# Performance work log

Measured on AMD Instinct MI355X. Metric: run time of the kernel, lower is better.

Reference implementation:

```python
import jax, jax.numpy as jnp
import numpy as np


def gcn_conv(x, W, b, src, dst):
    """PyG-style GCNConv: add self-loops, symmetric normalization, then scatter-add."""
    n = x.shape[0]
    loop = jnp.arange(n, dtype=src.dtype)
    s = jnp.concatenate([src, loop])  # [E+N]
    d = jnp.concatenate([dst, loop])
    deg = jax.ops.segment_sum(jnp.ones(s.shape[0], dtype=x.dtype), d, num_segments=n)
    dinv = jax.lax.rsqrt(jnp.maximum(deg, 1.0))  # deg >= 1 due to self-loops
    norm = dinv[s] * dinv[d]                     # [E+N]
    h = x @ W                                    # [N, out]
    msg = h[s] * norm[:, None]                   # gather + scale
    return jax.ops.segment_sum(msg, d, num_segments=n) + b


def setup_inputs() -> dict:
    key = jax.random.key(0)
    ks = jax.random.split(key, 8)
    N, E, IN, H, C = 50000, 800000, 128, 64, 16
    x = jax.random.normal(ks[0], (N, IN), dtype=jnp.float32)
    edge_index = jax.random.randint(ks[1], (2, E), 0, N, dtype=jnp.int32)
    def glorot(k, shp):
        fan_in, fan_out = shp
        lim = (6.0 / (fan_in + fan_out)) ** 0.5
        return jax.random.uniform(k, shp, jnp.float32, -lim, lim)
    return {
        "x": x,
        "edge_index": edge_index,
        "W1": glorot(ks[2], (IN, H)), "b1": jnp.zeros((H,), jnp.float32),
        "W2": glorot(ks[3], (H, H)),  "b2": jnp.zeros((H,), jnp.float32),
        "Wm1": glorot(ks[4], (2 * H, H)), "bm1": jnp.zeros((H,), jnp.float32),
        "Wm2": glorot(ks[5], (H, C)),     "bm2": jnp.zeros((C,), jnp.float32),
    }


def reference(x, edge_index, W1, b1, W2, b2, Wm1, bm1, Wm2, bm2):
    src, dst = edge_index[0], edge_index[1]
    h = jax.nn.relu(gcn_conv(x, W1, b1, src, dst))
    # dropout is identity in eval mode
    h = jax.nn.relu(gcn_conv(h, W2, b2, src, dst))
    ef = jnp.concatenate([h[src], h[dst]], axis=1)  # [E, 2H]
    z = jax.nn.relu(ef @ Wm1 + bm1)
    return z @ Wm2 + bm2  # [E, numClasses]
```

## Files before the change

### kernel.cpp

```cpp
#include <hip/hip_runtime.h>
#include <hip/hip_bf16.h>

__global__ __launch_bounds__(256) void k_deg(const int* __restrict__ dst, int* __restrict__ deg, int E) {
    int e = blockIdx.x * 256 + threadIdx.x;
    if (e < E) atomicAdd(&deg[dst[e]], 1);
}

__global__ __launch_bounds__(256) void k_scan_sum(const int* __restrict__ deg, int* __restrict__ bsum,
                                                  float* __restrict__ dinv, int N) {
    int n = blockIdx.x * 256 + threadIdx.x;
    int v = (n < N) ? deg[n] : 0;
    if (n < N) dinv[n] = rsqrtf((float)(v + 1));
    int r = v;
#pragma unroll
    for (int o = 32; o > 0; o >>= 1) r += __shfl_down(r, o, 64);
    __shared__ int sh[4];
    if ((threadIdx.x & 63) == 0) sh[threadIdx.x >> 6] = r;
    __syncthreads();
    if (threadIdx.x == 0) bsum[blockIdx.x] = sh[0] + sh[1] + sh[2] + sh[3];
}

__global__ __launch_bounds__(256) void k_scan_off(int* __restrict__ bsum, int nb) {
    __shared__ int sh[256];
    int t = threadIdx.x;
    sh[t] = (t < nb) ? bsum[t] : 0;
    __syncthreads();
    for (int o = 1; o < 256; o <<= 1) {
        int y = (t >= o) ? sh[t - o] : 0;
        __syncthreads();
        sh[t] += y;
        __syncthreads();
    }
    if (t < nb) bsum[t] = (t == 0) ? 0 : sh[t - 1];
}

__global__ __launch_bounds__(256) void k_scan_write(const int* __restrict__ deg, const int* __restrict__ boff,
                                                    int* __restrict__ row_start, int* __restrict__ cursor, int N) {
    int n = blockIdx.x * 256 + threadIdx.x;
    int t = threadIdx.x, lane = t & 63, w = t >> 6;
    int v = (n < N) ? deg[n] : 0;
    int x = v;
#pragma unroll
    for (int o = 1; o < 64; o <<= 1) {
        int y = __shfl_up(x, o, 64);
        if (lane >= o) x += y;
    }
    __shared__ int wsum[4];
    if (lane == 63) wsum[w] = x;
    __syncthreads();
    int wo = 0;
#pragma unroll
    for (int i = 0; i < 4; ++i) wo += (i < w) ? wsum[i] : 0;
    int excl = boff[blockIdx.x] + wo + x - v;
    if (n < N) { row_start[n] = excl; cursor[n] = excl; }
    if (n == N - 1) row_start[N] = excl + v;
}

template <bool PAIR>
__global__ __launch_bounds__(256) void k_fill(const int* __restrict__ src, const int* __restrict__ dst,
                                              int* __restrict__ cursor, void* __restrict__ item, int E) {
    int e = blockIdx.x * 256 + threadIdx.x;
    if (e < E) {
        int d = dst[e];
        int pos = atomicAdd(&cursor[d], 1);
        if (PAIR) ((int2*)item)[pos] = make_int2(src[e], e);
        else      ((int*)item)[pos] = e;
    }
}

__global__ __launch_bounds__(256) void k_dvec(const int* __restrict__ rowst, int* __restrict__ dvec, int N) {
    int w = threadIdx.x >> 6, lane = threadIdx.x & 63;
    int d = blockIdx.x * 4 + w;
    if (d >= N) return;
    int beg = rowst[d], end = rowst[d + 1];
    for (int k = beg + lane; k < end; k += 64) dvec[k] = d;
}

__global__ __launch_bounds__(256) void k_prep(const float* __restrict__ W1, const float* __restrict__ W2,
                                              const float* __restrict__ Wm2, const float* __restrict__ Wm1,
                                              float* __restrict__ W1T, float* __restrict__ W2T,
                                              float* __restrict__ Wm2T, float* __restrict__ WPQ,
                                              int IN, int H) {
    int i = blockIdx.x * 256 + threadIdx.x;
    int n1 = IN * H, n2 = H * H, n3 = H * 16, n4 = 2 * H * H;
    if (i < n1) {
        int r = i / H, c = i % H;
        W1T[(size_t)c * IN + r] = W1[(size_t)r * H + c];
    } else if ((i -= n1) < n2) {
        int r = i / H, c = i % H;
        W2T[(size_t)c * H + r] = W2[(size_t)r * H + c];
    } else if ((i -= n2) < n3) {
        int r = i / 16, c = i % 16;
        Wm2T[(size_t)c * H + r] = Wm2[(size_t)r * 16 + c];
    } else if ((i -= n3) < n4) {
        int j = i >> 6, k = i & 63;
        WPQ[i] = (j < 64) ? Wm1[k * 64 + j] : Wm1[(64 + k) * 64 + (j - 64)];
    }
}

template <int K, bool RELU, bool BIAS, bool SCALE>
__global__ __launch_bounds__(256) void k_mm_slice(const float* __restrict__ X,
                                                  const float* __restrict__ WT,
                                                  const float* __restrict__ bias,
                                                  const float* __restrict__ dinv,
                                                  float* __restrict__ Y, int N) {
    int n = blockIdx.x * 256 + threadIdx.x;
    int j0 = blockIdx.y * 16;
    int nc = n < N ? n : N - 1;
    const float* xr = X + (size_t)nc * K;
    const float* wr = WT + (size_t)j0 * K;
    float acc[16];
#pragma unroll
    for (int j = 0; j < 16; ++j) acc[j] = BIAS ? bias[j0 + j] : 0.f;
#pragma unroll 1
    for (int k0 = 0; k0 < K; k0 += 8) {
        float ef[8];
        *(float4*)(ef)     = *(const float4*)(xr + k0);
        *(float4*)(ef + 4) = *(const float4*)(xr + k0 + 4);
        if (RELU) {
#pragma unroll
            for (int kk = 0; kk < 8; ++kk) ef[kk] = fmaxf(ef[kk], 0.f);
        }
#pragma unroll
        for (int j = 0; j < 16; ++j) {
#pragma unroll
            for (int kk = 0; kk < 8; ++kk)
                acc[j] = fmaf(ef[kk], wr[j * K + k0 + kk], acc[j]);
        }
    }
    if (n < N) {
        if (SCALE) {
            float dn = dinv[n];
#pragma unroll
            for (int j = 0; j < 16; ++j) acc[j] *= dn;
        }
        float4* yp = (float4*)(Y + (size_t)n * 64 + j0);
#pragma unroll
        for (int q = 0; q < 4; ++q) yp[q] = *(float4*)(acc + q * 4);
    }
}

__global__ __launch_bounds__(256) void k_pq_slice(const float* __restrict__ A2,
                                                  const float* __restrict__ WPQ,
                                                  const float* __restrict__ bm1,
                                                  float* __restrict__ Pb, float* __restrict__ Qb, int N) {
    int n = blockIdx.x * 256 + threadIdx.x;
    int j0g = blockIdx.y * 16;
    bool isP = j0g < 64;
    int jo = isP ? j0g : j0g - 64;
    float* Y = isP ? Pb : Qb;
    int nc = n < N ? n : N - 1;
    const float* xr = A2 + (size_t)nc * 64;
    const float* wr = WPQ + (size_t)j0g * 64;
    float acc[16];
#pragma unroll
    for (int j = 0; j < 16; ++j) acc[j] = isP ? bm1[jo + j] : 0.f;
#pragma unroll 1
    for (int k0 = 0; k0 < 64; k0 += 8) {
        float ef[8];
        *(float4*)(ef)     = *(const float4*)(xr + k0);
        *(float4*)(ef + 4) = *(const float4*)(xr + k0 + 4);
#pragma unroll
        for (int kk = 0; kk < 8; ++kk) ef[kk] = fmaxf(ef[kk], 0.f);
#pragma unroll
        for (int j = 0; j < 16; ++j)
#pragma unroll
            for (int kk = 0; kk < 8; ++kk)
                acc[j] = fmaf(ef[kk], wr[j * 64 + k0 + kk], acc[j]);
    }
    if (n < N) {
        float4* yp = (float4*)(Y + (size_t)n * 64 + jo);
#pragma unroll
        for (int q = 0; q < 4; ++q) yp[q] = *(float4*)(acc + q * 4);
    }
}

template <bool PAIR>
__global__ __launch_bounds__(256) void k_gather(const float* __restrict__ hs, const float* __restrict__ dinv,
                                                const int* __restrict__ row_start, const void* __restrict__ item,
                                                const int* __restrict__ srcArr,
                                                const float* __restrict__ bias,
                                                float* __restrict__ a, int N) {
    int w = threadIdx.x >> 6, lane = threadIdx.x & 63;
    int d = blockIdx.x * 4 + w;
    if (d >= N) return;
    int beg = row_start[d], end = row_start[d + 1];
    float dd = dinv[d];
    float acc = hs[(size_t)d * 64 + lane];
    int k = beg;
    for (; k + 16 <= end; k += 16) {
        int ss[16];
        if (PAIR) {
            const int2* it = (const int2*)item;
#pragma unroll
            for (int u = 0; u < 16; ++u) ss[u] = it[k + u].x;
        } else {
            const int* eid = (const int*)item;
            int ee[16];
#pragma unroll
            for (int u = 0; u < 16; ++u) ee[u] = eid[k + u];
#pragma unroll
            for (int u = 0; u < 16; ++u) ss[u] = srcArr[ee[u]];
        }
        float v[16];
#pragma unroll
        for (int u = 0; u < 16; ++u) v[u] = hs[(size_t)ss[u] * 64 + lane];
#pragma unroll
        for (int u = 0; u < 16; ++u) acc += v[u];
    }
    for (; k + 8 <= end; k += 8) {
        int ss[8];
        if (PAIR) {
            const int2* it = (const int2*)item;
#pragma unroll
            for (int u = 0; u < 8; ++u) ss[u] = it[k + u].x;
        } else {
            const int* eid = (const int*)item;
            int ee[8];
#pragma unroll
            for (int u = 0; u < 8; ++u) ee[u] = eid[k + u];
#pragma unroll
            for (int u = 0; u < 8; ++u) ss[u] = srcArr[ee[u]];
        }
        float v[8];
#pragma unroll
        for (int u = 0; u < 8; ++u) v[u] = hs[(size_t)ss[u] * 64 + lane];
#pragma unroll
        for (int u = 0; u < 8; ++u) acc += v[u];
    }
    for (; k < end; ++k) {
        int s = PAIR ? ((const int2*)item)[k].x : srcArr[((const int*)item)[k]];
        acc += hs[(size_t)s * 64 + lane];
    }
    a[(size_t)d * 64 + lane] = fmaf(acc, dd, bias[lane]);
}

__global__ __launch_bounds__(256) void k_p_inplace(float* __restrict__ A2P,
                                                   const float* __restrict__ WPQ,
                                                   const float* __restrict__ bm1, int N) {
    int n = blockIdx.x * 256 + threadIdx.x;
    int nc = n < N ? n : N - 1;
    const float* xr = A2P + (size_t)nc * 64;
    float acc[64];
#pragma unroll
    for (int j = 0; j < 64; ++j) acc[j] = bm1[j];
#pragma unroll 1
    for (int k0 = 0; k0 < 64; k0 += 8) {
        float ef[8];
        *(float4*)(ef)     = *(const float4*)(xr + k0);
        *(float4*)(ef + 4) = *(const float4*)(xr + k0 + 4);
#pragma unroll
        for (int kk = 0; kk < 8; ++kk) ef[kk] = fmaxf(ef[kk], 0.f);
#pragma unroll
        for (int j = 0; j < 64; ++j)
#pragma unroll
            for (int kk = 0; kk < 8; ++kk)
                acc[j] = fmaf(ef[kk], WPQ[j * 64 + k0 + kk], acc[j]);
    }
    if (n < N) {
#pragma unroll
        for (int q = 0; q < 16; ++q)
            *(float4*)(A2P + (size_t)n * 64 + q * 4) = *(float4*)(acc + q * 4);
    }
}

__global__ __launch_bounds__(256) void k_edge_pq(const float* __restrict__ P,
                                                 const float* __restrict__ Q,
                                                 const int* __restrict__ src,
                                                 const int* __restrict__ dst,
                                                 const float* __restrict__ W2T,
                                                 const float* __restrict__ bm2,
                                                 float* __restrict__ out, int E) {
    int e = blockIdx.x * 256 + threadIdx.x;
    int ec = e < E ? e : E - 1;
    int s = src[ec], d = dst[ec];
    const float4* p4 = (const float4*)(P + (size_t)s * 64);
    const float4* q4 = (const float4*)(Q + (size_t)d * 64);
    float z[64];
#pragma unroll
    for (int c = 0; c < 16; ++c) {
        float4 a = p4[c], b = q4[c];
        z[c * 4 + 0] = fmaxf(a.x + b.x, 0.f);
        z[c * 4 + 1] = fmaxf(a.y + b.y, 0.f);
        z[c * 4 + 2] = fmaxf(a.z + b.z, 0.f);
        z[c * 4 + 3] = fmaxf(a.w + b.w, 0.f);
    }
    float o[16];
#pragma unroll
    for (int c = 0; c < 16; ++c) {
        float a = bm2[c];
#pragma unroll
        for (int j = 0; j < 64; ++j) a = fmaf(z[j], W2T[c * 64 + j], a);
        o[c] = a;
    }
    if (e < E) {
        float4* op = (float4*)(out + (size_t)e * 16);
#pragma unroll
        for (int q = 0; q < 4; ++q) op[q] = *(float4*)(o + q * 4);
    }
}

template <bool PAIR>
__global__ __launch_bounds__(256) void k_edge_csr(const float* __restrict__ P,
                                                  const float* __restrict__ Q,
                                                  const int* __restrict__ dvec,
                                                  const void* __restrict__ item,
                                                  const int* __restrict__ srcArr,
                                                  const float* __restrict__ W2T,
                                                  const float* __restrict__ bm2,
                                                  float* __restrict__ out, int E) {
    int i = blockIdx.x * 256 + threadIdx.x;
    int ic = i < E ? i : E - 1;
    int s, e;
    if (PAIR) {
        int2 pe = ((const int2*)item)[ic];
        s = pe.x; e = pe.y;
    } else {
        e = ((const int*)item)[ic];
        s = srcArr[e];
    }
    int d = dvec[ic];
    const float4* p4 = (const float4*)(P + (size_t)s * 64);
    const float4* q4 = (const float4*)(Q + (size_t)d * 64);
    float o[16];
#pragma unroll
    for (int t = 0; t < 16; ++t) o[t] = bm2[t];
#pragma unroll
    for (int cc = 0; cc < 16; ++cc) {
        float4 a = p4[cc], b = q4[cc];
        float z0 = fmaxf(a.x + b.x, 0.f);
        float z1 = fmaxf(a.y + b.y, 0.f);
        float z2 = fmaxf(a.z + b.z, 0.f);
        float z3 = fmaxf(a.w + b.w, 0.f);
#pragma unroll
        for (int t = 0; t < 16; ++t) {
            o[t] = fmaf(z0, W2T[t * 64 + cc * 4 + 0], o[t]);
            o[t] = fmaf(z1, W2T[t * 64 + cc * 4 + 1], o[t]);
            o[t] = fmaf(z2, W2T[t * 64 + cc * 4 + 2], o[t]);
            o[t] = fmaf(z3, W2T[t * 64 + cc * 4 + 3], o[t]);
        }
    }
    if (i < E) {
        float4* op = (float4*)(out + (size_t)e * 16);
#pragma unroll
        for (int q = 0; q < 4; ++q) op[q] = *(float4*)(o + q * 4);
    }
}

extern "C" void kernel_launch(void* const* d_in, const int* in_sizes, int n_in,
                              void* d_out, int out_size, void* d_ws, size_t ws_size,
                              hipStream_t stream) {
    const float* x   = (const float*)d_in[0];
    const int* ei    = (const int*)d_in[1];
    const float* W1  = (const float*)d_in[2];
    const float* b1  = (const float*)d_in[3];
    const float* W2  = (const float*)d_in[4];
    const float* b2  = (const float*)d_in[5];
    const float* Wm1 = (const float*)d_in[6];
    const float* bm1 = (const float*)d_in[7];
    const float* Wm2 = (const float*)d_in[8];
    const float* bm2 = (const float*)d_in[9];
    float* out = (float*)d_out;

    const int H  = in_sizes[3];
    const int IN = in_sizes[2] / H;
    const int N  = in_sizes[0] / IN;
    const int E  = in_sizes[1] / 2;
    const int* src = ei;
    const int* dst = ei + E;

    auto al = [](size_t b) { return (b + 255) & ~(size_t)255; };
    char* ws = (char*)d_ws;

    const size_t wb     = al((size_t)IN * H * 4) + al((size_t)H * H * 4) + al((size_t)2 * H * H * 4) + al((size_t)H * 16 * 4);
    const size_t rowstB = al(((size_t)N + 1) * 4);
    const size_t nodeB  = al((size_t)N * 64 * 4);
    const size_t pairB  = al((size_t)E * 8);
    const size_t eidB   = al((size_t)E * 4);
    const size_t needA  = wb + rowstB + pairB + 3 * nodeB;
    const size_t needB  = wb + rowstB + eidB  + 3 * nodeB;

    const int tier = (needA <= ws_size) ? 0 : (needB <= ws_size) ? 1 : 2;

    float *W1T, *W2T, *WPQ, *Wm2T, *bufB, *Qbuf, *Pbuf, *dinv;
    int *deg, *rowst, *cursor, *bsum;
    void* item;
    float* bufA = (float*)d_out;
    bool slicedP = true;

    size_t off = 0;
    auto alc = [&](size_t b) { void* p = ws + off; off += al(b); return p; };

    if (tier <= 1) {
        W1T  = (float*)alc((size_t)IN * H * 4);
        W2T  = (float*)alc((size_t)H * H * 4);
        WPQ  = (float*)alc((size_t)2 * H * H * 4);
        Wm2T = (float*)alc((size_t)H * 16 * 4);
        rowst = (int*)alc(((size_t)N + 1) * 4);
        item  = alc(tier == 0 ? (size_t)E * 8 : (size_t)E * 4);
        bufB = (float*)alc((size_t)N * 64 * 4);
        Qbuf = (float*)alc((size_t)N * 64 * 4);
        Pbuf = (float*)alc((size_t)N * 64 * 4);
        char* pz = (char*)Pbuf;
        dinv   = (float*)pz;
        deg    = (int*)(pz + al((size_t)N * 4));
        cursor = (int*)(pz + 2 * al((size_t)N * 4));
        bsum   = (int*)(pz + 3 * al((size_t)N * 4));
    } else {
        dinv = (float*)alc((size_t)N * 4);
        W1T  = (float*)alc((size_t)IN * H * 4);
        W2T  = (float*)alc((size_t)H * H * 4);
        WPQ  = (float*)alc((size_t)2 * H * H * 4);
        Wm2T = (float*)alc((size_t)H * 16 * 4);
        bufB = (float*)alc((size_t)N * 64 * 4);
        Qbuf = (float*)alc((size_t)N * 64 * 4);
        float* PbufSep = (float*)alc((size_t)N * 64 * 4);
        slicedP = (off <= ws_size);
        Pbuf = slicedP ? PbufSep : bufB;
        char* qz = (char*)Qbuf;
        size_t qo = 0;
        deg    = (int*)(qz + qo); qo += al((size_t)N * 4);
        rowst  = (int*)(qz + qo); qo += al(((size_t)N + 1) * 4);
        cursor = (int*)(qz + qo); qo += al((size_t)N * 4);
        bsum   = (int*)(qz + qo); qo += al(1024);
        item   = (void*)(qz + qo);
    }

    const int NBn = (N + 255) / 256;
    const int NBe = (E + 255) / 256;
    const int NG  = (N + 3) / 4;

    hipMemsetAsync(deg, 0, (size_t)N * sizeof(int), stream);
    k_deg<<<NBe, 256, 0, stream>>>(dst, deg, E);
    k_scan_sum<<<NBn, 256, 0, stream>>>(deg, bsum, dinv, N);
    k_scan_off<<<1, 256, 0, stream>>>(bsum, NBn);
    k_scan_write<<<NBn, 256, 0, stream>>>(deg, bsum, rowst, cursor, N);
    if (tier == 1) k_fill<false><<<NBe, 256, 0, stream>>>(src, dst, cursor, item, E);
    else           k_fill<true ><<<NBe, 256, 0, stream>>>(src, dst, cursor, item, E);

    const int prepElems = IN * H + H * H + H * 16 + 2 * H * H;
    k_prep<<<(prepElems + 255) / 256, 256, 0, stream>>>(W1, W2, Wm2, Wm1, W1T, W2T, Wm2T, WPQ, IN, H);

    const dim3 G4(NBn, 4);
    const dim3 G8(NBn, 8);

    k_mm_slice<128, false, false, true><<<G4, 256, 0, stream>>>(x, W1T, nullptr, dinv, bufA, N);
    if (tier == 1) k_gather<false><<<NG, 256, 0, stream>>>(bufA, dinv, rowst, item, src, b1, bufB, N);
    else           k_gather<true ><<<NG, 256, 0, stream>>>(bufA, dinv, rowst, item, src, b1, bufB, N);

    k_mm_slice<64, true, false, true><<<G4, 256, 0, stream>>>(bufB, W2T, nullptr, dinv, bufA, N);
    if (tier == 1) k_gather<false><<<NG, 256, 0, stream>>>(bufA, dinv, rowst, item, src, b2, bufB, N);
    else           k_gather<true ><<<NG, 256, 0, stream>>>(bufA, dinv, rowst, item, src, b2, bufB, N);

    if (tier <= 1) {
        k_pq_slice<<<G8, 256, 0, stream>>>(bufB, WPQ, bm1, Pbuf, Qbuf, N);
        int* dvec = (int*)bufB;
        k_dvec<<<NG, 256, 0, stream>>>(rowst, dvec, N);
        if (tier == 0) k_edge_csr<true ><<<NBe, 256, 0, stream>>>(Pbuf, Qbuf, dvec, item, src, Wm2T, bm2, out, E);
        else           k_edge_csr<false><<<NBe, 256, 0, stream>>>(Pbuf, Qbuf, dvec, item, src, Wm2T, bm2, out, E);
    } else {
        k_mm_slice<64, true, false, false><<<G4, 256, 0, stream>>>(bufB, WPQ + 64 * 64, nullptr, nullptr, Qbuf, N);
        if (slicedP) k_mm_slice<64, true, true, false><<<G4, 256, 0, stream>>>(bufB, WPQ, bm1, nullptr, Pbuf, N);
        else         k_p_inplace<<<NBn, 256, 0, stream>>>(bufB, WPQ, bm1, N);
        k_edge_pq<<<NBe, 256, 0, stream>>>(Pbuf, Qbuf, src, dst, Wm2T, bm2, out, E);
    }
}
```

Measured before the change: 411.9 us.

## Bucket CSR edges by source-node chunk to improve gather locality

```diff
diff --git a/kernel.cpp b/kernel.cpp
--- a/kernel.cpp
+++ b/kernel.cpp
@@ -1,44 +1,69 @@
 #include <hip/hip_runtime.h>
 #include <hip/hip_bf16.h>
 
-__global__ __launch_bounds__(256) void k_deg(const int* __restrict__ dst, int* __restrict__ deg, int E) {
+#define CHS 13
+
+__global__ __launch_bounds__(256) void k_deg(const int* __restrict__ src, const int* __restrict__ dst,
+                                             int* __restrict__ degc, int E, int N) {
     int e = blockIdx.x * 256 + threadIdx.x;
-    if (e < E) atomicAdd(&deg[dst[e]], 1);
-}
-
-__global__ __launch_bounds__(256) void k_scan_sum(const int* __restrict__ deg, int* __restrict__ bsum,
-                                                  float* __restrict__ dinv, int N) {
-    int n = blockIdx.x * 256 + threadIdx.x;
-    int v = (n < N) ? deg[n] : 0;
-    if (n < N) dinv[n] = rsqrtf((float)(v + 1));
-    int r = v;
-#pragma unroll
-    for (int o = 32; o > 0; o >>= 1) r += __shfl_down(r, o, 64);
+    if (e < E) {
+        int s = src[e], d = dst[e];
+        atomicAdd(&degc[(s >> CHS) * N + d], 1);
+    }
+}
+
+__global__ __launch_bounds__(256) void k_dinv(const int* __restrict__ degc, float* __restrict__ dinv,
+                                              int N, int NCH) {
+    int n = blockIdx.x * 256 + threadIdx.x;
+    if (n < N) {
+        int v = 0;
+        for (int c = 0; c < NCH; ++c) v += degc[c * N + n];
+        dinv[n] = rsqrtf((float)(v + 1));
+    }
+}
+
+__global__ __launch_bounds__(256) void k_scan_sum(const int* __restrict__ deg, int* __restrict__ bsum, int T) {
+    int n = blockIdx.x * 256 + threadIdx.x;
+    int v = (n < T) ? deg[n] : 0;
+#pragma unroll
+    for (int o = 32; o > 0; o >>= 1) v += __shfl_down(v, o, 64);
     __shared__ int sh[4];
-    if ((threadIdx.x & 63) == 0) sh[threadIdx.x >> 6] = r;
+    if ((threadIdx.x & 63) == 0) sh[threadIdx.x >> 6] = v;
     __syncthreads();
     if (threadIdx.x == 0) bsum[blockIdx.x] = sh[0] + sh[1] + sh[2] + sh[3];
 }
 
 __global__ __launch_bounds__(256) void k_scan_off(int* __restrict__ bsum, int nb) {
     __shared__ int sh[256];
+    __shared__ int carry_s;
     int t = threadIdx.x;
-    sh[t] = (t < nb) ? bsum[t] : 0;
+    if (t == 0) carry_s = 0;
     __syncthreads();
-    for (int o = 1; o < 256; o <<= 1) {
-        int y = (t >= o) ? sh[t - o] : 0;
+    for (int base = 0; base < nb; base += 256) {
+        int idx = base + t;
+        int v = (idx < nb) ? bsum[idx] : 0;
+        sh[t] = v;
         __syncthreads();
-        sh[t] += y;
+        for (int o = 1; o < 256; o <<= 1) {
+            int y = (t >= o) ? sh[t - o] : 0;
+            __syncthreads();
+            sh[t] += y;
+            __syncthreads();
+        }
+        int incl = sh[t];
+        int carry = carry_s;
+        if (idx < nb) bsum[idx] = carry + incl - v;
         __syncthreads();
-    }
-    if (t < nb) bsum[t] = (t == 0) ? 0 : sh[t - 1];
+        if (t == 255) carry_s = carry + incl;
+        __syncthreads();
+    }
 }
 
 __global__ __launch_bounds__(256) void k_scan_write(const int* __restrict__ deg, const int* __restrict__ boff,
-                                                    int* __restrict__ row_start, int* __restrict__ cursor, int N) {
+                                                    int* __restrict__ row_start, int* __restrict__ cursor, int T) {
     int n = blockIdx.x * 256 + threadIdx.x;
     int t = threadIdx.x, lane = t & 63, w = t >> 6;
-    int v = (n < N) ? deg[n] : 0;
+    int v = (n < T) ? deg[n] : 0;
     int x = v;
 #pragma unroll
     for (int o = 1; o < 64; o <<= 1) {
@@ -52,28 +77,29 @@
 #pragma unroll
     for (int i = 0; i < 4; ++i) wo += (i < w) ? wsum[i] : 0;
     int excl = boff[blockIdx.x] + wo + x - v;
-    if (n < N) { row_start[n] = excl; cursor[n] = excl; }
-    if (n == N - 1) row_start[N] = excl + v;
+    if (n < T) { row_start[n] = excl; cursor[n] = excl; }
+    if (n == T - 1) row_start[T] = excl + v;
 }
 
 template <bool PAIR>
 __global__ __launch_bounds__(256) void k_fill(const int* __restrict__ src, const int* __restrict__ dst,
-                                              int* __restrict__ cursor, void* __restrict__ item, int E) {
+                                              int* __restrict__ cursor, void* __restrict__ item, int E, int N) {
     int e = blockIdx.x * 256 + threadIdx.x;
     if (e < E) {
-        int d = dst[e];
-        int pos = atomicAdd(&cursor[d], 1);
-        if (PAIR) ((int2*)item)[pos] = make_int2(src[e], e);
+        int s = src[e], d = dst[e];
+        int pos = atomicAdd(&cursor[(s >> CHS) * N + d], 1);
+        if (PAIR) ((int2*)item)[pos] = make_int2(s, e);
         else      ((int*)item)[pos] = e;
     }
 }
 
-__global__ __launch_bounds__(256) void k_dvec(const int* __restrict__ rowst, int* __restrict__ dvec, int N) {
-    int w = threadIdx.x >> 6, lane = threadIdx.x & 63;
-    int d = blockIdx.x * 4 + w;
-    if (d >= N) return;
-    int beg = rowst[d], end = rowst[d + 1];
-    for (int k = beg + lane; k < end; k += 64) dvec[k] = d;
+__global__ __launch_bounds__(256) void k_dvec(const int* __restrict__ rowst, int* __restrict__ dvec,
+                                              int N, int T) {
+    int f = blockIdx.x * 256 + threadIdx.x;
+    if (f >= T) return;
+    int beg = rowst[f], end = rowst[f + 1];
+    int d = f % N;
+    for (int k = beg; k < end; ++k) dvec[k] = d;
 }
 
 __global__ __launch_bounds__(256) void k_prep(const float* __restrict__ W1, const float* __restrict__ W2,
@@ -177,60 +203,37 @@
 
 template <bool PAIR>
 __global__ __launch_bounds__(256) void k_gather(const float* __restrict__ hs, const float* __restrict__ dinv,
-                                                const int* __restrict__ row_start, const void* __restrict__ item,
+                                                const int* __restrict__ rowst, const void* __restrict__ item,
                                                 const int* __restrict__ srcArr,
                                                 const float* __restrict__ bias,
-                                                float* __restrict__ a, int N) {
+                                                float* __restrict__ a, int N, int NCH) {
     int w = threadIdx.x >> 6, lane = threadIdx.x & 63;
     int d = blockIdx.x * 4 + w;
     if (d >= N) return;
-    int beg = row_start[d], end = row_start[d + 1];
     float dd = dinv[d];
     float acc = hs[(size_t)d * 64 + lane];
-    int k = beg;
-    for (; k + 16 <= end; k += 16) {
-        int ss[16];
-        if (PAIR) {
-            const int2* it = (const int2*)item;
-#pragma unroll
-            for (int u = 0; u < 16; ++u) ss[u] = it[k + u].x;
-        } else {
-            const int* eid = (const int*)item;
-            int ee[16];
-#pragma unroll
-            for (int u = 0; u < 16; ++u) ee[u] = eid[k + u];
-#pragma unroll
-            for (int u = 0; u < 16; ++u) ss[u] = srcArr[ee[u]];
-        }
-        float v[16];
-#pragma unroll
-        for (int u = 0; u < 16; ++u) v[u] = hs[(size_t)ss[u] * 64 + lane];
-#pragma unroll
-        for (int u = 0; u < 16; ++u) acc += v[u];
-    }
-    for (; k + 8 <= end; k += 8) {
-        int ss[8];
-        if (PAIR) {
-            const int2* it = (const int2*)item;
-#pragma unroll
-            for (int u = 0; u < 8; ++u) ss[u] = it[k + u].x;
-        } else {
-            const int* eid = (const int*)item;
-            int ee[8];
-#pragma unroll
-            for (int u = 0; u < 8; ++u) ee[u] = eid[k + u];
-#pragma unroll
-            for (int u = 0; u < 8; ++u) ss[u] = srcArr[ee[u]];
-        }
-        float v[8];
-#pragma unroll
-        for (int u = 0; u < 8; ++u) v[u] = hs[(size_t)ss[u] * 64 + lane];
-#pragma unroll
-        for (int u = 0; u < 8; ++u) acc += v[u];
-    }
-    for (; k < end; ++k) {
-        int s = PAIR ? ((const int2*)item)[k].x : srcArr[((const int*)item)[k]];
-        acc += hs[(size_t)s * 64 + lane];
+    for (int c = 0; c < NCH; ++c) {
+        int f = c * N + d;
+        int k = rowst[f], kend = rowst[f + 1];
+        for (; k + 4 <= kend; k += 4) {
+            int s0, s1, s2, s3;
+            if (PAIR) {
+                const int2* it = (const int2*)item;
+                int2 p0 = it[k], p1 = it[k + 1], p2 = it[k + 2], p3 = it[k + 3];
+                s0 = p0.x; s1 = p1.x; s2 = p2.x; s3 = p3.x;
+            } else {
+                const int* eid = (const int*)item;
+                int e0 = eid[k], e1 = eid[k + 1], e2 = eid[k + 2], e3 = eid[k + 3];
+                s0 = srcArr[e0]; s1 = srcArr[e1]; s2 = srcArr[e2]; s3 = srcArr[e3];
+            }
+            float v0 = hs[(size_t)s0 * 64 + lane], v1 = hs[(size_t)s1 * 64 + lane];
+            float v2 = hs[(size_t)s2 * 64 + lane], v3 = hs[(size_t)s3 * 64 + lane];
+            acc += v0; acc += v1; acc += v2; acc += v3;
+        }
+        for (; k < kend; ++k) {
+            int s = PAIR ? ((const int2*)item)[k].x : srcArr[((const int*)item)[k]];
+            acc += hs[(size_t)s * 64 + lane];
+        }
     }
     a[(size_t)d * 64 + lane] = fmaf(acc, dd, bias[lane]);
 }
@@ -369,11 +372,14 @@
     const int* src = ei;
     const int* dst = ei + E;
 
+    const int NCH = (N + (1 << CHS) - 1) >> CHS;
+    const int TOT = NCH * N;
+
     auto al = [](size_t b) { return (b + 255) & ~(size_t)255; };
     char* ws = (char*)d_ws;
 
     const size_t wb     = al((size_t)IN * H * 4) + al((size_t)H * H * 4) + al((size_t)2 * H * H * 4) + al((size_t)H * 16 * 4);
-    const size_t rowstB = al(((size_t)N + 1) * 4);
+    const size_t rowstB = al(((size_t)TOT + 1) * 4);
     const size_t nodeB  = al((size_t)N * 64 * 4);
     const size_t pairB  = al((size_t)E * 8);
     const size_t eidB   = al((size_t)E * 4);
@@ -383,7 +389,7 @@
     const int tier = (needA <= ws_size) ? 0 : (needB <= ws_size) ? 1 : 2;
 
     float *W1T, *W2T, *WPQ, *Wm2T, *bufB, *Qbuf, *Pbuf, *dinv;
-    int *deg, *rowst, *cursor, *bsum;
+    int *degc, *rowst, *cursor, *bsum;
     void* item;
     float* bufA = (float*)d_out;
     bool slicedP = true;
@@ -396,16 +402,17 @@
         W2T  = (float*)alc((size_t)H * H * 4);
         WPQ  = (float*)alc((size_t)2 * H * H * 4);
         Wm2T = (float*)alc((size_t)H * 16 * 4);
-        rowst = (int*)alc(((size_t)N + 1) * 4);
+        rowst = (int*)alc(((size_t)TOT + 1) * 4);
         item  = alc(tier == 0 ? (size_t)E * 8 : (size_t)E * 4);
         bufB = (float*)alc((size_t)N * 64 * 4);
         Qbuf = (float*)alc((size_t)N * 64 * 4);
         Pbuf = (float*)alc((size_t)N * 64 * 4);
         char* pz = (char*)Pbuf;
-        dinv   = (float*)pz;
-        deg    = (int*)(pz + al((size_t)N * 4));
-        cursor = (int*)(pz + 2 * al((size_t)N * 4));
-        bsum   = (int*)(pz + 3 * al((size_t)N * 4));
+        size_t po = 0;
+        dinv   = (float*)(pz + po); po += al((size_t)N * 4);
+        degc   = (int*)(pz + po);   po += al((size_t)TOT * 4);
+        cursor = (int*)(pz + po);   po += al((size_t)TOT * 4);
+        bsum   = (int*)(pz + po);   po += al(8192);
     } else {
         dinv = (float*)alc((size_t)N * 4);
         W1T  = (float*)alc((size_t)IN * H * 4);
@@ -419,24 +426,26 @@
         Pbuf = slicedP ? PbufSep : bufB;
         char* qz = (char*)Qbuf;
         size_t qo = 0;
-        deg    = (int*)(qz + qo); qo += al((size_t)N * 4);
-        rowst  = (int*)(qz + qo); qo += al(((size_t)N + 1) * 4);
-        cursor = (int*)(qz + qo); qo += al((size_t)N * 4);
-        bsum   = (int*)(qz + qo); qo += al(1024);
+        degc   = (int*)(qz + qo); qo += al((size_t)TOT * 4);
+        rowst  = (int*)(qz + qo); qo += al(((size_t)TOT + 1) * 4);
+        cursor = (int*)(qz + qo); qo += al((size_t)TOT * 4);
+        bsum   = (int*)(qz + qo); qo += al(8192);
         item   = (void*)(qz + qo);
     }
 
     const int NBn = (N + 255) / 256;
     const int NBe = (E + 255) / 256;
+    const int NBt = (TOT + 255) / 256;
     const int NG  = (N + 3) / 4;
 
-    hipMemsetAsync(deg, 0, (size_t)N * sizeof(int), stream);
-    k_deg<<<NBe, 256, 0, stream>>>(dst, deg, E);
-    k_scan_sum<<<NBn, 256, 0, stream>>>(deg, bsum, dinv, N);
-    k_scan_off<<<1, 256, 0, stream>>>(bsum, NBn);
-    k_scan_write<<<NBn, 256, 0, stream>>>(deg, bsum, rowst, cursor, N);
-    if (tier == 1) k_fill<false><<<NBe, 256, 0, stream>>>(src, dst, cursor, item, E);
-    else           k_fill<true ><<<NBe, 256, 0, stream>>>(src, dst, cursor, item, E);
+    hipMemsetAsync(degc, 0, (size_t)TOT * sizeof(int), stream);
+    k_deg<<<NBe, 256, 0, stream>>>(src, dst, degc, E, N);
+    k_dinv<<<NBn, 256, 0, stream>>>(degc, dinv, N, NCH);
+    k_scan_sum<<<NBt, 256, 0, stream>>>(degc, bsum, TOT);
+    k_scan_off<<<1, 256, 0, stream>>>(bsum, NBt);
+    k_scan_write<<<NBt, 256, 0, stream>>>(degc, bsum, rowst, cursor, TOT);
+    if (tier == 0) k_fill<true ><<<NBe, 256, 0, stream>>>(src, dst, cursor, item, E, N);
+    else           k_fill<false><<<NBe, 256, 0, stream>>>(src, dst, cursor, item, E, N);
 
     const int prepElems = IN * H + H * H + H * 16 + 2 * H * H;
     k_prep<<<(prepElems + 255) / 256, 256, 0, stream>>>(W1, W2, Wm2, Wm1, W1T, W2T, Wm2T, WPQ, IN, H);
@@ -445,17 +454,17 @@
     const dim3 G8(NBn, 8);
 
     k_mm_slice<128, false, false, true><<<G4, 256, 0, stream>>>(x, W1T, nullptr, dinv, bufA, N);
-    if (tier == 1) k_gather<false><<<NG, 256, 0, stream>>>(bufA, dinv, rowst, item, src, b1, bufB, N);
-    else           k_gather<true ><<<NG, 256, 0, stream>>>(bufA, dinv, rowst, item, src, b1, bufB, N);
+    if (tier == 0) k_gather<true ><<<NG, 256, 0, stream>>>(bufA, dinv, rowst, item, src, b1, bufB, N, NCH);
+    else           k_gather<false><<<NG, 256, 0, stream>>>(bufA, dinv, rowst, item, src, b1, bufB, N, NCH);
 
     k_mm_slice<64, true, false, true><<<G4, 256, 0, stream>>>(bufB, W2T, nullptr, dinv, bufA, N);
-    if (tier == 1) k_gather<false><<<NG, 256, 0, stream>>>(bufA, dinv, rowst, item, src, b2, bufB, N);
-    else           k_gather<true ><<<NG, 256, 0, stream>>>(bufA, dinv, rowst, item, src, b2, bufB, N);
+    if (tier == 0) k_gather<true ><<<NG, 256, 0, stream>>>(bufA, dinv, rowst, item, src, b2, bufB, N, NCH);
+    else           k_gather<false><<<NG, 256, 0, stream>>>(bufA, dinv, rowst, item, src, b2, bufB, N, NCH);
 
     if (tier <= 1) {
         k_pq_slice<<<G8, 256, 0, stream>>>(bufB, WPQ, bm1, Pbuf, Qbuf, N);
         int* dvec = (int*)bufB;
-        k_dvec<<<NG, 256, 0, stream>>>(rowst, dvec, N);
+        k_dvec<<<NBt, 256, 0, stream>>>(rowst, dvec, N, TOT);
         if (tier == 0) k_edge_csr<true ><<<NBe, 256, 0, stream>>>(Pbuf, Qbuf, dvec, item, src, Wm2T, bm2, out, E);
         else           k_edge_csr<false><<<NBe, 256, 0, stream>>>(Pbuf, Qbuf, dvec, item, src, Wm2T, bm2, out, E);
     } else {
```

Measured after the change: 495.6 us. +20.3%, slower.
